# Kernel optimization log

Hardware: AMD Instinct MI355X
Metric: run time of the kernel (lower is better)

The kernel has to match this reference:

```python
import jax, jax.numpy as jnp
import numpy as np

TOL = 1e-3

def centered_grid(h, w):
    x = jnp.arange(w, dtype=jnp.float32) - (w - 1) / 2.0
    y = jnp.arange(h, dtype=jnp.float32) - (h - 1) / 2.0
    X = jnp.broadcast_to(x[None, :], (h, w))
    Y = jnp.broadcast_to(y[:, None], (h, w))
    return X, Y

def param_to_H(p):
    B = p.shape[0]
    z = jnp.zeros((B, 1, 1), dtype=p.dtype)
    return jnp.concatenate([p, z], axis=1).reshape(B, 3, 3) + jnp.eye(3, dtype=p.dtype)

def grid_sample_bilinear(A, xn, yn):
    # torch grid_sample, mode='bilinear', align_corners=False, padding_mode='zeros'
    B, k, h, w = A.shape
    ix = ((xn + 1.0) * w - 1.0) / 2.0
    iy = ((yn + 1.0) * h - 1.0) / 2.0
    x0 = jnp.floor(ix).astype(jnp.int32); x1 = x0 + 1
    y0 = jnp.floor(iy).astype(jnp.int32); y1 = y0 + 1
    wx1 = ix - x0.astype(ix.dtype); wx0 = 1.0 - wx1
    wy1 = iy - y0.astype(iy.dtype); wy0 = 1.0 - wy1
    def gather(xi, yi):
        valid = ((xi >= 0) & (xi <= w - 1) & (yi >= 0) & (yi <= h - 1)).astype(A.dtype)
        xc = jnp.clip(xi, 0, w - 1); yc = jnp.clip(yi, 0, h - 1)
        vals = jax.vmap(lambda a, yy, xx: a[:, yy, xx])(A, yc, xc)  # [B,k,h,w]
        return vals * valid[:, None, :, :]
    out = (gather(x0, y0) * (wx0 * wy0)[:, None]
           + gather(x1, y0) * (wx1 * wy0)[:, None]
           + gather(x0, y1) * (wx0 * wy1)[:, None]
           + gather(x1, y1) * (wx1 * wy1)[:, None])
    return out

def warp_hmg(img, p):
    B, k, h, w = img.shape
    X, Y = centered_grid(h, w)
    xy = jnp.stack([X.reshape(-1), Y.reshape(-1), jnp.ones(h * w, jnp.float32)], 0)  # [3,hw]
    H = param_to_H(p)
    xyw = jnp.einsum('bij,jn->bin', H, xy)
    Xw = (xyw[:, 0] / xyw[:, 2]).reshape(B, h, w) + (w - 1) / 2.0
    Yw = (xyw[:, 1] / xyw[:, 2]).reshape(B, h, w) + (h - 1) / 2.0
    xn = Xw / ((w - 1) / 2.0) - 1.0
    yn = Yw / ((h - 1) / 2.0) - 1.0
    Q = grid_sample_bilinear(img, xn, yn)
    mask = ((xn > -1 + 2.0 / w) & (xn < 1 - 2.0 / w)
            & (yn > -1 + 2.0 / h) & (yn < 1 - 2.0 / h)).astype(img.dtype)
    return Q, mask

def image_gradients(img):
    # central differences with replicate padding (matches GradientBatch)
    px = jnp.pad(img, ((0, 0), (0, 0), (0, 0), (1, 1)), mode='edge')
    dx = 0.5 * (px[..., 2:] - px[..., :-2])
    py = jnp.pad(img, ((0, 0), (0, 0), (1, 1), (0, 0)), mode='edge')
    dy = 0.5 * (py[..., 2:, :] - py[..., :-2, :])
    return dx, dy

def compute_dIdp(gx, gy):
    B, k, h, w = gx.shape
    X, Y = centered_grid(h, w)
    Xf = jnp.tile(X.reshape(-1), k)  # [k*h*w]
    Yf = jnp.tile(Y.reshape(-1), k)
    gx = gx.reshape(B, k * h * w)
    gy = gy.reshape(B, k * h * w)
    cols = [Xf * gx, Yf * gx, gx, Xf * gy, Yf * gy, gy,
            -Xf * Xf * gx - Xf * Yf * gy, -Xf * Yf * gx - Yf * Yf * gy]
    return jnp.stack(cols, axis=2)  # [B, k*h*w, 8]

def deeplk_forward(img, temp, max_itr):
    Fi, Ft = img, temp
    B, k, h, w = Ft.shape
    gx, gy = image_gradients(Ft)
    dIdp = compute_dIdp(gx, gy)                      # [B, N, 8]
    invH = jnp.linalg.inv(jnp.einsum('bni,bnj->bij', dIdp, dIdp))  # [B,8,8]
    invH_dIdp = jnp.einsum('bij,bnj->bin', invH, dIdp)             # [B,8,N]
    p0 = jnp.zeros((B, 8, 1), jnp.float32)
    dp0 = jnp.ones((B, 8, 1), jnp.float32)

    def step(carry, _):
        p, dp = carry
        Fi_warp, mask = warp_hmg(Fi, p)
        r = (Fi_warp - Ft * mask[:, None]).reshape(B, -1, 1)
        dp_new = jnp.einsum('bin,bnj->bij', invH_dIdp, r)
        dp_new = dp_new.at[:, 6:8, 0].set(0.0)
        cond = (jnp.linalg.norm(dp, axis=1, keepdims=True) > TOL).astype(p.dtype)
        dp2 = cond * dp_new  # per-sample gate: once converged dp stays 0 (matches torch while-loop)
        return (p - dp2, dp2), None

    (p, _), _ = jax.lax.scan(step, (p0, dp0), None, length=int(max_itr))
    return p, param_to_H(p)

def setup_inputs() -> dict:
    key = jax.random.key(0)
    k1, k2 = jax.random.split(key)
    img = jax.random.normal(k1, (16, 3, 256, 256), jnp.float32)
    temp = jax.random.normal(k2, (16, 3, 256, 256), jnp.float32)
    return {"img": img, "temp": temp, "max_itr": 20}

def reference(img, temp, max_itr):
    return deeplk_forward(img, temp, max_itr)
```

## Files before the change

kernel.cpp:

```cpp
#include <hip/hip_runtime.h>

#define BATCH 16
#define KCH 3
#define IH 256
#define IW 256
#define NPIX (IH*IW)
#define NITER 20
#define HCH 64
#define CH 32
#define TPBF 256
#define TPBM 1024
#define NBLK (BATCH*CH)

#define AGENT __HIP_MEMORY_SCOPE_AGENT

struct Ws {
    float  hess_part[BATCH][HCH][36];
    double invH[BATCH][64];
    double s0[BATCH][HCH][8];
    double s_part[2][BATCH][CH][8];
    double sfb[2][BATCH][HCH][8];
    double p[2][BATCH][8];
    double dpn2[2][BATCH];
    int    cnt[NITER][BATCH][32];
};

__device__ __forceinline__ double aload_d(const double* p) {
    return __hip_atomic_load(p, __ATOMIC_RELAXED, AGENT);
}
__device__ __forceinline__ void astore_d(double* p, double v) {
    __hip_atomic_store(p, v, __ATOMIC_RELAXED, AGENT);
}

__device__ __forceinline__ void pixel_accum(const float* __restrict__ I,
                                            const float* __restrict__ T,
                                            int x, int y,
                                            float h00, float h01, float h02,
                                            float h10, float h11, float h12,
                                            float* acc8, float* acc36, bool do_hess) {
    const float XL = -1.f + 2.f / IW, XH = 1.f - 2.f / IW;
    const float YL = -1.f + 2.f / IH, YH = 1.f - 2.f / IH;
    float X = (float)x - 127.5f, Y = (float)y - 127.5f;

    float Xw = (h00 * X + h01 * Y + h02) + 127.5f;
    float Yw = (h10 * X + h11 * Y + h12) + 127.5f;
    float xn = Xw / 127.5f - 1.f;
    float yn = Yw / 127.5f - 1.f;

    float ix = ((xn + 1.f) * (float)IW - 1.f) * 0.5f;
    float iy = ((yn + 1.f) * (float)IH - 1.f) * 0.5f;
    float fx0 = floorf(ix), fy0 = floorf(iy);
    int x0 = (int)fx0, y0 = (int)fy0;
    int x1 = x0 + 1, y1 = y0 + 1;
    float wx1 = ix - fx0, wx0 = 1.f - wx1;
    float wy1 = iy - fy0, wy0 = 1.f - wy1;

    bool vx0 = (x0 >= 0) && (x0 <= IW - 1), vx1 = (x1 >= 0) && (x1 <= IW - 1);
    bool vy0 = (y0 >= 0) && (y0 <= IH - 1), vy1 = (y1 >= 0) && (y1 <= IH - 1);
    int xc0 = min(max(x0, 0), IW - 1), xc1 = min(max(x1, 0), IW - 1);
    int yc0 = min(max(y0, 0), IH - 1), yc1 = min(max(y1, 0), IH - 1);

    float w00 = (wx0 * wy0) * ((vx0 && vy0) ? 1.f : 0.f);
    float w10 = (wx1 * wy0) * ((vx1 && vy0) ? 1.f : 0.f);
    float w01 = (wx0 * wy1) * ((vx0 && vy1) ? 1.f : 0.f);
    float w11 = (wx1 * wy1) * ((vx1 && vy1) ? 1.f : 0.f);

    float mask = (xn > XL && xn < XH && yn > YL && yn < YH) ? 1.f : 0.f;

#pragma unroll
    for (int c = 0; c < KCH; c++) {
        const float* Ic = I + c * NPIX;
        const float* Tc = T + c * NPIX;
        float v00 = Ic[yc0 * IW + xc0];
        float v10 = Ic[yc0 * IW + xc1];
        float v01 = Ic[yc1 * IW + xc0];
        float v11 = Ic[yc1 * IW + xc1];
        float Q = v00 * w00 + v10 * w10 + v01 * w01 + v11 * w11;
        float r = Q - Tc[y * IW + x] * mask;
        float gx = 0.5f * (Tc[y * IW + min(x + 1, IW - 1)] - Tc[y * IW + max(x - 1, 0)]);
        float gy = 0.5f * (Tc[min(y + 1, IH - 1) * IW + x] - Tc[max(y - 1, 0) * IW + x]);
        float gxr = gx * r, gyr = gy * r;
        float ur = X * gxr + Y * gyr;
        acc8[0] += X * gxr;
        acc8[1] += Y * gxr;
        acc8[2] += gxr;
        acc8[3] += X * gyr;
        acc8[4] += Y * gyr;
        acc8[5] += gyr;
        acc8[6] -= X * ur;
        acc8[7] -= Y * ur;
        if (do_hess) {
            float d[8];
            d[0] = X * gx; d[1] = Y * gx; d[2] = gx;
            d[3] = X * gy; d[4] = Y * gy; d[5] = gy;
            d[6] = -X * X * gx - X * Y * gy;
            d[7] = -X * Y * gx - Y * Y * gy;
            int idx = 0;
#pragma unroll
            for (int i = 0; i < 8; i++)
#pragma unroll
                for (int j = i; j < 8; j++) { acc36[idx] += d[i] * d[j]; idx++; }
        }
    }
}

__global__ __launch_bounds__(TPBF) void k_first(const float* __restrict__ img,
                                                const float* __restrict__ temp, Ws* ws) {
    const int b = blockIdx.y, chunk = blockIdx.x, t = threadIdx.x;
    const int lane = t & 63, wave = t >> 6;
    float acc8[8], acc36[36];
#pragma unroll
    for (int i = 0; i < 8; i++) acc8[i] = 0.f;
#pragma unroll
    for (int i = 0; i < 36; i++) acc36[i] = 0.f;
    const float* I = img + (size_t)b * KCH * NPIX;
    const float* T = temp + (size_t)b * KCH * NPIX;

#pragma unroll
    for (int pp = 0; pp < 4; ++pp)
        pixel_accum(I, T, t, chunk * 4 + pp, 1.f, 0.f, 0.f, 0.f, 1.f, 0.f,
                    acc8, acc36, true);

#pragma unroll
    for (int i = 0; i < 36; i++) {
        float v = acc36[i];
        for (int o = 32; o > 0; o >>= 1) v += __shfl_xor(v, o, 64);
        acc36[i] = v;
    }
#pragma unroll
    for (int i = 0; i < 8; i++) {
        float v = acc8[i];
        for (int o = 32; o > 0; o >>= 1) v += __shfl_xor(v, o, 64);
        acc8[i] = v;
    }
    __shared__ float red36[4][36];
    __shared__ float red8[4][8];
    if (lane == 0) {
#pragma unroll
        for (int i = 0; i < 36; i++) red36[wave][i] = acc36[i];
#pragma unroll
        for (int i = 0; i < 8; i++) red8[wave][i] = acc8[i];
    }
    __syncthreads();
    if (t < 36)
        ws->hess_part[b][chunk][t] = red36[0][t] + red36[1][t] + red36[2][t] + red36[3][t];
    if (t < 8)
        ws->s0[b][chunk][t] =
            (double)(red8[0][t] + red8[1][t] + red8[2][t] + red8[3][t]);
}

__global__ __launch_bounds__(1024) void k_invert(Ws* ws) {
    const int t = threadIdx.x;
    {
        int* c = &ws->cnt[0][0][0];
        const int total = NITER * BATCH * 32;
        for (int i = t; i < total; i += 1024) c[i] = 0;
    }
    const int b = t >> 6, lane = t & 63;
    double hv = 0.0;
    if (lane < 36) {
        for (int c = 0; c < HCH; c++) hv += (double)ws->hess_part[b][c][lane];
    }
    const int ii = lane >> 3, jj = lane & 7;
    const int a = min(ii, jj), bb = max(ii, jj);
    const int pidx = a * 8 - a * (a - 1) / 2 + (bb - a);
    double Mv = __shfl(hv, pidx, 64);
    double Av = (ii == jj) ? 1.0 : 0.0;
#pragma unroll
    for (int k = 0; k < 8; k++) {
        double pivd = __shfl(Mv, k * 8 + k, 64);
        double inv = 1.0 / pivd;
        double rM = __shfl(Mv, k * 8 + jj, 64) * inv;
        double rA = __shfl(Av, k * 8 + jj, 64) * inv;
        double fac = __shfl(Mv, ii * 8 + k, 64);
        if (ii == k) { Mv = rM; Av = rA; }
        else         { Mv -= fac * rM; Av -= fac * rA; }
    }
    ws->invH[b][lane] = Av;
}

__device__ __forceinline__ void batchbar(Ws* ws, int it, int b) {
    asm volatile("s_waitcnt vmcnt(0)" ::: "memory");
    __syncthreads();
    if (threadIdx.x == 0) {
        __hip_atomic_fetch_add(&ws->cnt[it][b][0], 1, __ATOMIC_RELAXED, AGENT);
        while (__hip_atomic_load(&ws->cnt[it][b][0], __ATOMIC_RELAXED, AGENT) < CH)
            __builtin_amdgcn_s_sleep(4);
    }
    __syncthreads();
    asm volatile("" ::: "memory");
}

__global__ __launch_bounds__(TPBM, 8) void mega_loop(const float* __restrict__ img,
                                                     const float* __restrict__ temp,
                                                     Ws* ws, float* __restrict__ out) {
    const int bid = blockIdx.x;
    const int b = bid & 15;
    const int chunk = bid >> 4;
    const int t = threadIdx.x;
    const int lane = t & 63, wave = t >> 6;
    const int x = t & 255, yrow = t >> 8;

    __shared__ float red8[16][8];

    const float* I = img + (size_t)b * KCH * NPIX;
    const float* T = temp + (size_t)b * KCH * NPIX;

    double ir[8];
#pragma unroll
    for (int j = 0; j < 8; j++) ir[j] = ws->invH[b][(lane & 7) * 8 + j];

    float tcv[2][KCH], gxv[2][KCH], gyv[2][KCH];
#pragma unroll
    for (int pp = 0; pp < 2; ++pp) {
        const int y = chunk * 8 + yrow * 2 + pp;
        const int ym = max(y - 1, 0), yp = min(y + 1, IH - 1);
        const int xm = max(x - 1, 0), xp = min(x + 1, IW - 1);
#pragma unroll
        for (int c = 0; c < KCH; c++) {
            const float* Tc = T + c * NPIX;
            tcv[pp][c] = Tc[y * IW + x];
            gxv[pp][c] = 0.5f * (Tc[y * IW + xp] - Tc[y * IW + xm]);
            gyv[pp][c] = 0.5f * (Tc[yp * IW + x] - Tc[ym * IW + x]);
        }
    }

    const float S = 256.0f / 255.0f;
    const float Xc = (float)x - 127.5f;
    const float Y0 = (float)(chunk * 8 + yrow * 2) - 127.5f;

    double p_reg = 0.0, dpn2 = 8.0;
    for (int it = 1; it <= NITER; ++it) {
        {
            const int j = lane & 7, c_lo = lane >> 3;
            double sv = 0.0;
            if (it == 1) {
#pragma unroll
                for (int m = 0; m < 8; m++)
                    sv += aload_d(&ws->s0[b][c_lo + 8 * m][j]);
            } else {
                const double* sp = &ws->s_part[(it - 1) & 1][b][0][0];
#pragma unroll
                for (int m = 0; m < 4; m++)
                    sv += aload_d(sp + (c_lo + 8 * m) * 8 + j);
            }
            sv += __shfl_xor(sv, 8, 64);
            sv += __shfl_xor(sv, 16, 64);
            sv += __shfl_xor(sv, 32, 64);
            double dp = 0.0;
#pragma unroll
            for (int jj = 0; jj < 8; jj++)
                dp += ir[jj] * __shfl(sv, jj, 64);
            double d = (lane < 6 && dpn2 > 1e-6) ? dp : 0.0;
            double n2 = d * d;
            n2 += __shfl_xor(n2, 1, 64);
            n2 += __shfl_xor(n2, 2, 64);
            n2 += __shfl_xor(n2, 4, 64);
            p_reg -= d;
            dpn2 = n2;
        }
        if (it == NITER) break;

        float pf[8];
#pragma unroll
        for (int jj = 0; jj < 8; jj++) pf[jj] = (float)__shfl(p_reg, jj, 64);
        const float h00 = 1.f + pf[0], h01 = pf[1], h02 = pf[2];
        const float h10 = pf[3], h11 = 1.f + pf[4], h12 = pf[5];

        const float ix0 = (h00 * Xc + h01 * Y0 + h02 + 127.5f) * S - 0.5f;
        const float iy0 = (h10 * Xc + h11 * Y0 + h12 + 127.5f) * S - 0.5f;
        const float dix = h01 * S, diy = h11 * S;

        float G1 = 0.f, G1Y = 0.f, G2 = 0.f, G2Y = 0.f, G2YY = 0.f;

#pragma unroll
        for (int pp = 0; pp < 2; ++pp) {
            const float Y = Y0 + (float)pp;
            const float ix = ix0 + (float)pp * dix;
            const float iy = iy0 + (float)pp * diy;

            float fx0 = floorf(ix), fy0 = floorf(iy);
            int x0 = (int)fx0, y0 = (int)fy0;
            int x1 = x0 + 1, y1 = y0 + 1;
            float wx1 = ix - fx0, wx0 = 1.f - wx1;
            float wy1 = iy - fy0, wy0 = 1.f - wy1;

            bool vx0 = (x0 >= 0) && (x0 <= IW - 1), vx1 = (x1 >= 0) && (x1 <= IW - 1);
            bool vy0 = (y0 >= 0) && (y0 <= IH - 1), vy1 = (y1 >= 0) && (y1 <= IH - 1);
            int xc0 = min(max(x0, 0), IW - 1), xc1 = min(max(x1, 0), IW - 1);
            int yc0 = min(max(y0, 0), IH - 1), yc1 = min(max(y1, 0), IH - 1);

            float w00 = (wx0 * wy0) * ((vx0 && vy0) ? 1.f : 0.f);
            float w10 = (wx1 * wy0) * ((vx1 && vy0) ? 1.f : 0.f);
            float w01 = (wx0 * wy1) * ((vx0 && vy1) ? 1.f : 0.f);
            float w11 = (wx1 * wy1) * ((vx1 && vy1) ? 1.f : 0.f);

            float mask = (ix > 0.5f && ix < 254.5f && iy > 0.5f && iy < 254.5f)
                         ? 1.f : 0.f;
            const float Y2 = Y * Y;

#pragma unroll
            for (int c = 0; c < KCH; c++) {
                const float* Ic = I + c * NPIX;
                float v00 = Ic[yc0 * IW + xc0];
                float v10 = Ic[yc0 * IW + xc1];
                float v01 = Ic[yc1 * IW + xc0];
                float v11 = Ic[yc1 * IW + xc1];
                float Q = v00 * w00 + v10 * w10 + v01 * w01 + v11 * w11;
                float r = Q - tcv[pp][c] * mask;
                float gxr = gxv[pp][c] * r, gyr = gyv[pp][c] * r;
                G1  += gxr;
                G1Y += Y * gxr;
                G2  += gyr;
                G2Y += Y * gyr;
                G2YY += Y2 * gyr;
            }
        }

        float acc8[8];
        acc8[0] = Xc * G1;
        acc8[1] = G1Y;
        acc8[2] = G1;
        acc8[3] = Xc * G2;
        acc8[4] = G2Y;
        acc8[5] = G2;
        acc8[6] = -Xc * (Xc * G1 + G2Y);
        acc8[7] = -(Xc * G1Y + G2YY);

#pragma unroll
        for (int i = 0; i < 8; i++) {
            float v = acc8[i];
            for (int o = 32; o > 0; o >>= 1) v += __shfl_xor(v, o, 64);
            acc8[i] = v;
        }
        if (lane == 0) {
#pragma unroll
            for (int i = 0; i < 8; i++) red8[wave][i] = acc8[i];
        }
        __syncthreads();
        if (t < 8) {
            float tot = 0.f;
#pragma unroll
            for (int w = 0; w < 16; w++) tot += red8[w][t];
            astore_d(&ws->s_part[it & 1][b][chunk][t], (double)tot);
        }
        batchbar(ws, it, b);
    }

    if (chunk == 0 && wave == 0) {
        if (lane < 8) {
            out[b * 8 + lane] = (float)p_reg;
            out[128 + b * 9 + lane] =
                (float)(p_reg + ((lane == 0 || lane == 4) ? 1.0 : 0.0));
        }
        if (lane == 8) out[128 + b * 9 + 8] = 1.0f;
    }
}

__device__ __forceinline__ double do_update_ws(const Ws* ws, int b, int it, int lane,
                                               double* n2_out) {
    const int j = lane & 7, c_lo = lane >> 3;
    const double* base = (it == 1) ? &ws->s0[b][0][0]
                                   : &ws->sfb[(it - 1) & 1][b][0][0];
    double sv = 0.0;
#pragma unroll
    for (int m = 0; m < 8; m++) sv += base[(c_lo + 8 * m) * 8 + j];
    sv += __shfl_xor(sv, 8, 64);
    sv += __shfl_xor(sv, 16, 64);
    sv += __shfl_xor(sv, 32, 64);
    const double* row = &ws->invH[b][(lane & 7) * 8];
    double dp = 0.0;
#pragma unroll
    for (int jj = 0; jj < 8; jj++) dp += row[jj] * __shfl(sv, jj, 64);
    double p_prev = 0.0, dpn2_prev = 8.0;
    if (it > 1) {
        if (lane < 8) p_prev = ws->p[(it - 1) & 1][b][lane];
        dpn2_prev = ws->dpn2[(it - 1) & 1][b];
    }
    double d = (lane < 6 && dpn2_prev > 1e-6) ? dp : 0.0;
    double n2 = d * d;
    n2 += __shfl_xor(n2, 1, 64);
    n2 += __shfl_xor(n2, 2, 64);
    n2 += __shfl_xor(n2, 4, 64);
    *n2_out = n2;
    return p_prev - d;
}

__global__ __launch_bounds__(TPBF) void k_iter(const float* __restrict__ img,
                                               const float* __restrict__ temp,
                                               Ws* ws, int it) {
    const int b = blockIdx.y, chunk = blockIdx.x, t = threadIdx.x;
    const int lane = t & 63, wave = t >> 6;
    double n2;
    double p_cur = do_update_ws(ws, b, it, lane, &n2);
    float pf[8];
#pragma unroll
    for (int jj = 0; jj < 8; jj++) pf[jj] = (float)__shfl(p_cur, jj, 64);
    if (chunk == 0 && wave == 0) {
        if (lane < 8) ws->p[it & 1][b][lane] = p_cur;
        if (lane == 0) ws->dpn2[it & 1][b] = n2;
    }
    float acc8[8];
#pragma unroll
    for (int i = 0; i < 8; i++) acc8[i] = 0.f;
    const float* I = img + (size_t)b * KCH * NPIX;
    const float* T = temp + (size_t)b * KCH * NPIX;
#pragma unroll
    for (int pp = 0; pp < 4; ++pp)
        pixel_accum(I, T, t, chunk * 4 + pp,
                    1.f + pf[0], pf[1], pf[2], pf[3], 1.f + pf[4], pf[5],
                    acc8, nullptr, false);
#pragma unroll
    for (int i = 0; i < 8; i++) {
        float v = acc8[i];
        for (int o = 32; o > 0; o >>= 1) v += __shfl_xor(v, o, 64);
        acc8[i] = v;
    }
    __shared__ float red8[4][8];
    if (lane == 0) {
#pragma unroll
        for (int i = 0; i < 8; i++) red8[wave][i] = acc8[i];
    }
    __syncthreads();
    if (t < 8)
        ws->sfb[it & 1][b][chunk][t] =
            (double)(red8[0][t] + red8[1][t] + red8[2][t] + red8[3][t]);
}

__global__ __launch_bounds__(1024) void k_out(Ws* ws, float* __restrict__ out) {
    const int t = threadIdx.x;
    const int b = t >> 6, lane = t & 63;
    double n2;
    double p_fin = do_update_ws(ws, b, NITER, lane, &n2);
    if (lane < 8) {
        out[b * 8 + lane] = (float)p_fin;
        out[128 + b * 9 + lane] =
            (float)(p_fin + ((lane == 0 || lane == 4) ? 1.0 : 0.0));
    }
    if (lane == 8) out[128 + b * 9 + 8] = 1.0f;
}

extern "C" void kernel_launch(void* const* d_in, const int* in_sizes, int n_in,
                              void* d_out, int out_size, void* d_ws, size_t ws_size,
                              hipStream_t stream) {
    const float* img  = (const float*)d_in[0];
    const float* temp = (const float*)d_in[1];
    Ws* ws = (Ws*)d_ws;
    float* out = (float*)d_out;

    k_first<<<dim3(HCH, BATCH), TPBF, 0, stream>>>(img, temp, ws);
    k_invert<<<1, 1024, 0, stream>>>(ws);

    int dev = 0, nCU = 0, maxB = 0;
    hipGetDevice(&dev);
    hipDeviceGetAttribute(&nCU, hipDeviceAttributeMultiprocessorCount, dev);
    hipError_t e = hipOccupancyMaxActiveBlocksPerMultiprocessor(
        &maxB, (const void*)mega_loop, TPBM, 0);
    const bool coop_ok = (e == hipSuccess) && ((long)maxB * nCU >= NBLK);

    if (coop_ok) {
        void* args[] = {(void*)&img, (void*)&temp, (void*)&ws, (void*)&out};
        hipLaunchCooperativeKernel((void*)mega_loop, dim3(NBLK), dim3(TPBM), args, 0,
                                   stream);
    } else {
        for (int it = 1; it < NITER; ++it)
            k_iter<<<dim3(HCH, BATCH), TPBF, 0, stream>>>(img, temp, ws, it);
        k_out<<<1, 1024, 0, stream>>>(ws, out);
    }
}
```

Baseline: 220.0 us.

## Use workgroup-scope atomics for per-batch barrier when all blocks share an XCD

Each block records its XCC id, then all blocks pass a global barrier. Each block then checks whether every block of its batch runs on the same XCD. If so, the per-iteration batch barrier and partial-sum exchange use workgroup-scope atomics and plain stores, aiming to keep traffic in the local L2 instead of going agent-wide. This adds an extra grid-wide barrier at kernel start and relies on the hardware dispatch placing a batch's blocks on one XCD. Workgroup scope across different CUs is a weak coherence guarantee, so correctness depends on the shared L2 behaviour.

```diff
diff --git a/kernel.cpp b/kernel.cpp
--- a/kernel.cpp
+++ b/kernel.cpp
@@ -13,6 +13,7 @@
 #define NBLK (BATCH*CH)
 
 #define AGENT __HIP_MEMORY_SCOPE_AGENT
+#define WG    __HIP_MEMORY_SCOPE_WORKGROUP
 
 struct Ws {
     float  hess_part[BATCH][HCH][36];
@@ -23,6 +24,8 @@
     double p[2][BATCH][8];
     double dpn2[2][BATCH];
     int    cnt[NITER][BATCH][32];
+    int    gbar[32];
+    int    xcd[NBLK];
 };
 
 __device__ __forceinline__ double aload_d(const double* p) {
@@ -153,7 +156,7 @@
     const int t = threadIdx.x;
     {
         int* c = &ws->cnt[0][0][0];
-        const int total = NITER * BATCH * 32;
+        const int total = NITER * BATCH * 32 + 32;
         for (int i = t; i < total; i += 1024) c[i] = 0;
     }
     const int b = t >> 6, lane = t & 63;
@@ -179,13 +182,19 @@
     ws->invH[b][lane] = Av;
 }
 
-__device__ __forceinline__ void batchbar(Ws* ws, int it, int b) {
+__device__ __forceinline__ void batchbar(Ws* ws, int it, int b, bool fast) {
     asm volatile("s_waitcnt vmcnt(0)" ::: "memory");
     __syncthreads();
     if (threadIdx.x == 0) {
-        __hip_atomic_fetch_add(&ws->cnt[it][b][0], 1, __ATOMIC_RELAXED, AGENT);
-        while (__hip_atomic_load(&ws->cnt[it][b][0], __ATOMIC_RELAXED, AGENT) < CH)
-            __builtin_amdgcn_s_sleep(4);
+        if (fast) {
+            __hip_atomic_fetch_add(&ws->cnt[it][b][0], 1, __ATOMIC_RELAXED, WG);
+            while (__hip_atomic_fetch_add(&ws->cnt[it][b][0], 0, __ATOMIC_RELAXED, WG) < CH)
+                __builtin_amdgcn_s_sleep(2);
+        } else {
+            __hip_atomic_fetch_add(&ws->cnt[it][b][0], 1, __ATOMIC_RELAXED, AGENT);
+            while (__hip_atomic_load(&ws->cnt[it][b][0], __ATOMIC_RELAXED, AGENT) < CH)
+                __builtin_amdgcn_s_sleep(4);
+        }
     }
     __syncthreads();
     asm volatile("" ::: "memory");
@@ -206,6 +215,30 @@
     const float* I = img + (size_t)b * KCH * NPIX;
     const float* T = temp + (size_t)b * KCH * NPIX;
 
+    {
+        int xcc = 0;
+        asm volatile("s_getreg_b32 %0, hwreg(HW_REG_XCC_ID)" : "=s"(xcc));
+        if (t == 0)
+            __hip_atomic_store(&ws->xcd[bid], xcc, __ATOMIC_RELAXED, AGENT);
+    }
+    asm volatile("s_waitcnt vmcnt(0)" ::: "memory");
+    __syncthreads();
+    if (t == 0) {
+        __hip_atomic_fetch_add(&ws->gbar[0], 1, __ATOMIC_RELAXED, AGENT);
+        while (__hip_atomic_load(&ws->gbar[0], __ATOMIC_RELAXED, AGENT) < NBLK)
+            __builtin_amdgcn_s_sleep(2);
+    }
+    __syncthreads();
+    bool fast;
+    {
+        int myx = 0;
+        if (lane < CH)
+            myx = __hip_atomic_load(&ws->xcd[(lane << 4) | b], __ATOMIC_RELAXED, AGENT);
+        int ref = __shfl(myx, 0, 64);
+        bool same = (lane < CH) ? (myx == ref) : true;
+        fast = __all(same);
+    }
+
     double ir[8];
 #pragma unroll
     for (int j = 0; j < 8; j++) ir[j] = ws->invH[b][(lane & 7) * 8 + j];
@@ -239,10 +272,17 @@
                 for (int m = 0; m < 8; m++)
                     sv += aload_d(&ws->s0[b][c_lo + 8 * m][j]);
             } else {
-                const double* sp = &ws->s_part[(it - 1) & 1][b][0][0];
-#pragma unroll
-                for (int m = 0; m < 4; m++)
-                    sv += aload_d(sp + (c_lo + 8 * m) * 8 + j);
+                double* sp = &ws->s_part[(it - 1) & 1][b][0][0];
+                if (fast) {
+#pragma unroll
+                    for (int m = 0; m < 4; m++)
+                        sv += __hip_atomic_fetch_add(sp + (c_lo + 8 * m) * 8 + j,
+                                                     0.0, __ATOMIC_RELAXED, WG);
+                } else {
+#pragma unroll
+                    for (int m = 0; m < 4; m++)
+                        sv += aload_d(sp + (c_lo + 8 * m) * 8 + j);
+                }
             }
             sv += __shfl_xor(sv, 8, 64);
             sv += __shfl_xor(sv, 16, 64);
@@ -342,9 +382,12 @@
             float tot = 0.f;
 #pragma unroll
             for (int w = 0; w < 16; w++) tot += red8[w][t];
-            astore_d(&ws->s_part[it & 1][b][chunk][t], (double)tot);
-        }
-        batchbar(ws, it, b);
+            if (fast)
+                ws->s_part[it & 1][b][chunk][t] = (double)tot;
+            else
+                astore_d(&ws->s_part[it & 1][b][chunk][t], (double)tot);
+        }
+        batchbar(ws, it, b, fast);
     }
 
     if (chunk == 0 && wave == 0) {
```

Result: no change. 219.9 us (-0.1%).

## Replace per-batch all-to-all barrier with leader-based arrive/go flag protocol

Applied to the files above, without the earlier changes.

Swaps the counter-based all-blocks barrier for a leader scheme. Chunk 0 of each batch polls per-chunk arrival flags, reduces the partial sums, computes the parameter update and broadcasts the float params plus a go flag to each follower chunk. Followers spin only on their own go flag, which removes the contended atomic counter and the redundant per-block update math. It also pads s_part to 16 doubles per chunk to avoid cache-line sharing, at the cost of a serial dependency through the leader block.

```diff
diff --git a/kernel.cpp b/kernel.cpp
--- a/kernel.cpp
+++ b/kernel.cpp
@@ -18,17 +18,31 @@
     float  hess_part[BATCH][HCH][36];
     double invH[BATCH][64];
     double s0[BATCH][HCH][8];
-    double s_part[2][BATCH][CH][8];
+    double s_part[2][BATCH][CH][16];
+    float  pfb[BATCH][CH][32];
+    int    arrive[BATCH][CH][32];
+    int    goflag[BATCH][CH][32];
     double sfb[2][BATCH][HCH][8];
     double p[2][BATCH][8];
     double dpn2[2][BATCH];
-    int    cnt[NITER][BATCH][32];
 };
 
 __device__ __forceinline__ double aload_d(const double* p) {
     return __hip_atomic_load(p, __ATOMIC_RELAXED, AGENT);
 }
 __device__ __forceinline__ void astore_d(double* p, double v) {
+    __hip_atomic_store(p, v, __ATOMIC_RELAXED, AGENT);
+}
+__device__ __forceinline__ float aload_f(const float* p) {
+    return __hip_atomic_load(p, __ATOMIC_RELAXED, AGENT);
+}
+__device__ __forceinline__ void astore_f(float* p, float v) {
+    __hip_atomic_store(p, v, __ATOMIC_RELAXED, AGENT);
+}
+__device__ __forceinline__ int aload_i(const int* p) {
+    return __hip_atomic_load(p, __ATOMIC_RELAXED, AGENT);
+}
+__device__ __forceinline__ void astore_i(int* p, int v) {
     __hip_atomic_store(p, v, __ATOMIC_RELAXED, AGENT);
 }
 
@@ -152,9 +166,10 @@
 __global__ __launch_bounds__(1024) void k_invert(Ws* ws) {
     const int t = threadIdx.x;
     {
-        int* c = &ws->cnt[0][0][0];
-        const int total = NITER * BATCH * 32;
-        for (int i = t; i < total; i += 1024) c[i] = 0;
+        int* a = &ws->arrive[0][0][0];
+        int* g = &ws->goflag[0][0][0];
+        const int total = BATCH * CH * 32;
+        for (int i = t; i < total; i += 1024) { a[i] = 0; g[i] = 0; }
     }
     const int b = t >> 6, lane = t & 63;
     double hv = 0.0;
@@ -177,18 +192,6 @@
         else         { Mv -= fac * rM; Av -= fac * rA; }
     }
     ws->invH[b][lane] = Av;
-}
-
-__device__ __forceinline__ void batchbar(Ws* ws, int it, int b) {
-    asm volatile("s_waitcnt vmcnt(0)" ::: "memory");
-    __syncthreads();
-    if (threadIdx.x == 0) {
-        __hip_atomic_fetch_add(&ws->cnt[it][b][0], 1, __ATOMIC_RELAXED, AGENT);
-        while (__hip_atomic_load(&ws->cnt[it][b][0], __ATOMIC_RELAXED, AGENT) < CH)
-            __builtin_amdgcn_s_sleep(4);
-    }
-    __syncthreads();
-    asm volatile("" ::: "memory");
 }
 
 __global__ __launch_bounds__(TPBM, 8) void mega_loop(const float* __restrict__ img,
@@ -200,8 +203,10 @@
     const int t = threadIdx.x;
     const int lane = t & 63, wave = t >> 6;
     const int x = t & 255, yrow = t >> 8;
+    const bool noti = (chunk == 0);
 
     __shared__ float red8[16][8];
+    __shared__ float pf_sh[8];
 
     const float* I = img + (size_t)b * KCH * NPIX;
     const float* T = temp + (size_t)b * KCH * NPIX;
@@ -230,8 +235,9 @@
     const float Y0 = (float)(chunk * 8 + yrow * 2) - 127.5f;
 
     double p_reg = 0.0, dpn2 = 8.0;
-    for (int it = 1; it <= NITER; ++it) {
-        {
+
+    for (int it = 1; it < NITER; ++it) {
+        if (noti && wave == 0) {
             const int j = lane & 7, c_lo = lane >> 3;
             double sv = 0.0;
             if (it == 1) {
@@ -239,10 +245,16 @@
                 for (int m = 0; m < 8; m++)
                     sv += aload_d(&ws->s0[b][c_lo + 8 * m][j]);
             } else {
+                const int need = it - 1;
+                for (;;) {
+                    int av = (lane < CH) ? aload_i(&ws->arrive[b][lane][0]) : need;
+                    if (__all(av >= need)) break;
+                    __builtin_amdgcn_s_sleep(1);
+                }
                 const double* sp = &ws->s_part[(it - 1) & 1][b][0][0];
 #pragma unroll
                 for (int m = 0; m < 4; m++)
-                    sv += aload_d(sp + (c_lo + 8 * m) * 8 + j);
+                    sv += aload_d(sp + (c_lo + 8 * m) * 16 + j);
             }
             sv += __shfl_xor(sv, 8, 64);
             sv += __shfl_xor(sv, 16, 64);
@@ -258,12 +270,32 @@
             n2 += __shfl_xor(n2, 4, 64);
             p_reg -= d;
             dpn2 = n2;
-        }
-        if (it == NITER) break;
+
+            float pfl[8];
+#pragma unroll
+            for (int jj = 0; jj < 8; jj++) pfl[jj] = (float)__shfl(p_reg, jj, 64);
+            if (lane < CH) {
+#pragma unroll
+                for (int jj = 0; jj < 8; jj++)
+                    astore_f(&ws->pfb[b][lane][jj], pfl[jj]);
+            }
+            asm volatile("s_waitcnt vmcnt(0)" ::: "memory");
+            if (lane >= 1 && lane < CH)
+                astore_i(&ws->goflag[b][lane][0], it);
+            if (lane < 8) pf_sh[lane] = pfl[lane];
+        } else if (!noti && wave == 0) {
+            if (lane == 0) {
+                while (aload_i(&ws->goflag[b][chunk][0]) < it)
+                    __builtin_amdgcn_s_sleep(1);
+            }
+            float pv = (lane < 8) ? aload_f(&ws->pfb[b][chunk][lane]) : 0.f;
+            if (lane < 8) pf_sh[lane] = pv;
+        }
+        __syncthreads();
 
         float pf[8];
 #pragma unroll
-        for (int jj = 0; jj < 8; jj++) pf[jj] = (float)__shfl(p_reg, jj, 64);
+        for (int jj = 0; jj < 8; jj++) pf[jj] = pf_sh[jj];
         const float h00 = 1.f + pf[0], h01 = pf[1], h02 = pf[2];
         const float h10 = pf[3], h11 = 1.f + pf[4], h12 = pf[5];
 
@@ -344,10 +376,33 @@
             for (int w = 0; w < 16; w++) tot += red8[w][t];
             astore_d(&ws->s_part[it & 1][b][chunk][t], (double)tot);
         }
-        batchbar(ws, it, b);
-    }
-
-    if (chunk == 0 && wave == 0) {
+        asm volatile("s_waitcnt vmcnt(0)" ::: "memory");
+        __syncthreads();
+        if (t == 0) astore_i(&ws->arrive[b][chunk][0], it);
+    }
+
+    if (noti && wave == 0) {
+        const int j = lane & 7, c_lo = lane >> 3;
+        const int need = NITER - 1;
+        for (;;) {
+            int av = (lane < CH) ? aload_i(&ws->arrive[b][lane][0]) : need;
+            if (__all(av >= need)) break;
+            __builtin_amdgcn_s_sleep(1);
+        }
+        const double* sp = &ws->s_part[(NITER - 1) & 1][b][0][0];
+        double sv = 0.0;
+#pragma unroll
+        for (int m = 0; m < 4; m++)
+            sv += aload_d(sp + (c_lo + 8 * m) * 16 + j);
+        sv += __shfl_xor(sv, 8, 64);
+        sv += __shfl_xor(sv, 16, 64);
+        sv += __shfl_xor(sv, 32, 64);
+        double dp = 0.0;
+#pragma unroll
+        for (int jj = 0; jj < 8; jj++)
+            dp += ir[jj] * __shfl(sv, jj, 64);
+        double d = (lane < 6 && dpn2 > 1e-6) ? dp : 0.0;
+        p_reg -= d;
         if (lane < 8) {
             out[b * 8 + lane] = (float)p_reg;
             out[128 + b * 9 + lane] =
```

Result: no change. 221.1 us (+0.5%).
